# Performance work log

Hardware: AMD Instinct MI355X
Metric: run time of the kernel (lower is better)

The kernel has to match this reference:

```python
import jax, jax.numpy as jnp
import numpy as np

NUM_STUDENTS = 50000
NUM_PROBLEMS = 10000
EMBED_DIM = 64
NNZ = 3200000


def _spmm(rows, cols, vals, x, num_out):
    # out[r] = sum_{edges e with rows[e]==r} vals[e] * x[cols[e]]
    msgs = vals[:, None] * x[cols]  # [nnz, d]
    return jax.ops.segment_sum(msgs, rows, num_segments=num_out)


def setup_inputs() -> dict:
    key = jax.random.key(0)
    ks = jax.random.split(key, 8)
    return {
        "student_embeds": jax.random.normal(ks[0], (NUM_STUDENTS, EMBED_DIM), jnp.float32),
        "problem_embeds": jax.random.normal(ks[1], (NUM_PROBLEMS, EMBED_DIM), jnp.float32),
        "a_rows": jax.random.randint(ks[2], (NNZ,), 0, NUM_STUDENTS, jnp.int32),
        "a_cols": jax.random.randint(ks[3], (NNZ,), 0, NUM_PROBLEMS, jnp.int32),
        "a_vals": jax.random.uniform(ks[4], (NNZ,), jnp.float32),
        "ia_rows": jax.random.randint(ks[5], (NNZ,), 0, NUM_STUDENTS, jnp.int32),
        "ia_cols": jax.random.randint(ks[6], (NNZ,), 0, NUM_PROBLEMS, jnp.int32),
        "ia_vals": jax.random.uniform(ks[7], (NNZ,), jnp.float32),
    }


def reference(student_embeds, problem_embeds, a_rows, a_cols, a_vals,
              ia_rows, ia_cols, ia_vals):
    num_students = student_embeds.shape[0]
    num_problems = problem_embeds.shape[0]
    # a_matrix @ problem_embeds
    student_embeds_c = _spmm(a_rows, a_cols, a_vals, problem_embeds, num_students)
    # a_matrix.T @ student_embeds (swap roles of rows/cols)
    problem_embeds_c = _spmm(a_cols, a_rows, a_vals, student_embeds, num_problems)
    student_embeds_ic = _spmm(ia_rows, ia_cols, ia_vals, problem_embeds, num_students)
    problem_embeds_ic = _spmm(ia_cols, ia_rows, ia_vals, student_embeds, num_problems)
    return (student_embeds_c, student_embeds_ic, problem_embeds_c, problem_embeds_ic)
```

## Files before the change

kernel.cpp:

```cpp
#include <hip/hip_runtime.h>
#include <hip/hip_bf16.h>

#define NBMAX 256
#define TILE  4096
#define KPT   16
#define BINSMAX 512

__device__ __forceinline__ int seg8(unsigned r, unsigned mult8) {
    return (int)__umulhi(r, mult8);
}

__global__ __launch_bounds__(256) void hist_all(
        const int* __restrict__ k0, const int* __restrict__ k1,
        const int* __restrict__ k2, const int* __restrict__ k3,
        int* __restrict__ gcnt4, int nnz, int rsh_s, int rsh_p) {
    __shared__ int h[NBMAX];
    int dir = blockIdx.x & 3;
    const int* key = (dir == 0) ? k0 : (dir == 1) ? k1 : (dir == 2) ? k2 : k3;
    int rsh = (dir & 1) ? rsh_p : rsh_s;
    h[threadIdx.x] = 0;
    __syncthreads();
    int ch = blockIdx.x >> 2, nch = gridDim.x >> 2;
    for (int i = ch * 256 + threadIdx.x; i < nnz; i += nch * 256)
        atomicAdd(&h[key[i] >> rsh], 1);
    __syncthreads();
    int v = h[threadIdx.x];
    if (v) atomicAdd(&gcnt4[dir * NBMAX + threadIdx.x], v);
}

__global__ __launch_bounds__(256) void scan_all(
        const int* __restrict__ gcnt4, int* __restrict__ boffs4,
        int* __restrict__ bcur4, int nb_s, int nb_p, int nnz,
        int* __restrict__ offsE, int* __restrict__ offsO, int NS, int NP8) {
    __shared__ int tmp[NBMAX];
    int dir = blockIdx.x, tid = threadIdx.x;
    int nb = (dir & 1) ? nb_p : nb_s;
    int v = (tid < nb) ? gcnt4[dir * NBMAX + tid] : 0;
    tmp[tid] = v;
    __syncthreads();
    for (int off = 1; off < NBMAX; off <<= 1) {
        int t = (tid >= off) ? tmp[tid - off] : 0;
        __syncthreads();
        tmp[tid] += t;
        __syncthreads();
    }
    if (tid < nb) {
        int e = tmp[tid] - v;
        boffs4[dir * (NBMAX + 1) + tid] = e;
        bcur4[dir * NBMAX + tid] = e;
    }
    if (tid == 0) boffs4[dir * (NBMAX + 1) + nb] = nnz;
    if (dir == 0 && tid == 0) { offsE[NS] = nnz; offsO[NP8] = nnz; }
}

__global__ __launch_bounds__(256) void staged_scatter(
        const int* __restrict__ key, const int* __restrict__ other,
        const float* __restrict__ vals, int* __restrict__ cursor,
        uint2* __restrict__ edges, int nnz, int rsh) {
    __shared__ int lhist[NBMAX], lofs[NBMAX], lbase[NBMAX];
    __shared__ uint2 stage[TILE];
    __shared__ int   sslot[TILE];
    int tid = threadIdx.x;
    int lmask = (1 << rsh) - 1;
    int ntiles = (nnz + TILE - 1) / TILE;
    for (int tile = blockIdx.x; tile < ntiles; tile += gridDim.x) {
        int tbeg = tile * TILE;
        int n = nnz - tbeg; if (n > TILE) n = TILE;
        lhist[tid] = 0;
        __syncthreads();
        int myb[KPT], myr[KPT]; unsigned myo[KPT]; float myv[KPT];
        #pragma unroll
        for (int k = 0; k < KPT; ++k) {
            int s = k * 256 + tid;
            if (s < n) {
                int i = tbeg + s;
                int ky = key[i];
                myb[k] = ky >> rsh;
                myo[k] = (unsigned)other[i] | ((unsigned)(ky & lmask) << 16);
                myv[k] = vals[i];
                myr[k] = atomicAdd(&lhist[myb[k]], 1);
            } else myb[k] = -1;
        }
        __syncthreads();
        int h = lhist[tid];
        lofs[tid] = h;
        __syncthreads();
        for (int off = 1; off < NBMAX; off <<= 1) {
            int t = (tid >= off) ? lofs[tid - off] : 0;
            __syncthreads();
            lofs[tid] += t;
            __syncthreads();
        }
        lofs[tid] -= h;
        if (h > 0) lbase[tid] = atomicAdd(&cursor[tid], h);
        __syncthreads();
        #pragma unroll
        for (int k = 0; k < KPT; ++k) {
            if (myb[k] >= 0) {
                int ls = lofs[myb[k]] + myr[k];
                stage[ls] = make_uint2(myo[k], __float_as_uint(myv[k]));
                sslot[ls] = lbase[myb[k]] + myr[k];
            }
        }
        __syncthreads();
        #pragma unroll
        for (int k = 0; k < KPT; ++k) {
            int s = k * 256 + tid;
            if (s < n) edges[sslot[s]] = stage[s];
        }
        __syncthreads();
    }
}

__global__ __launch_bounds__(512) void row_scatter2(
        const uint2* __restrict__ e1, uint2* __restrict__ e2,
        const int* __restrict__ boffs, int* __restrict__ offs,
        int odd, int nb, int rsh, int nrows, unsigned mult8) {
    __shared__ int cnt[BINSMAX * 8];
    __shared__ int tot[512];
    __shared__ int lcur[BINSMAX];
    int tid = threadIdx.x;
    int g = blockIdx.x;
    int x = g & 7;
    int sk = (g >> 3) & 7;
    int bi = g >> 6;
    int b = x + 8 * bi;
    if (b >= nb) return;
    int bins = odd ? (8 << rsh) : (1 << rsh);
    int beg = boffs[b], end = boffs[b + 1];
    int len = end - beg;
    for (int i = tid; i < BINSMAX * 8; i += 512) cnt[i] = 0;
    __syncthreads();
    int per = (len + 7) >> 3;
    if (len > 0) {
        for (int i = beg + tid; i < end; i += 512) {
            uint2 e = e1[i];
            int lrow = (int)(e.x >> 16);
            int bin = odd ? (lrow * 8 + seg8(e.x & 0xFFFFu, mult8)) : lrow;
            int sl = (i - beg) / per;
            atomicAdd(&cnt[bin * 8 + sl], 1);
        }
    }
    __syncthreads();
    int own = 0;
    if (tid < bins) {
        #pragma unroll
        for (int j = 0; j < 8; ++j) own += cnt[tid * 8 + j];
    }
    tot[tid] = (tid < bins) ? own : 0;
    __syncthreads();
    for (int off = 1; off < 512; off <<= 1) {
        int t = (tid >= off) ? tot[tid - off] : 0;
        __syncthreads();
        tot[tid] += t;
        __syncthreads();
    }
    if (tid < bins) {
        int fineoff = tot[tid] - own;
        int basej = 0;
        for (int j = 0; j < sk; ++j) basej += cnt[tid * 8 + j];
        lcur[tid] = beg + fineoff + basej;
        if (sk == 0) {
            if (!odd) {
                int row = (b << rsh) + tid;
                if (row < nrows) offs[row] = beg + fineoff;
            } else {
                int row = (b << rsh) + (tid >> 3);
                if (row < nrows) offs[(row << 3) + (tid & 7)] = beg + fineoff;
            }
        }
    }
    __syncthreads();
    int lo = beg + sk * per;
    int hi = lo + per; if (hi > end) hi = end;
    for (int i = lo + tid; i < hi; i += 512) {
        uint2 e = e1[i];
        int lrow = (int)(e.x >> 16);
        int bin = odd ? (lrow * 8 + seg8(e.x & 0xFFFFu, mult8)) : lrow;
        int slot = atomicAdd(&lcur[bin], 1);
        e2[slot] = make_uint2(e.x & 0xFFFFu, e.y);
    }
}

__device__ __forceinline__ float4 gather_row4(
        int beg, int end, const uint2* __restrict__ edges,
        const float* __restrict__ x, int lane) {
    int q = lane >> 4, l16 = lane & 15;
    float4 acc = make_float4(0.f, 0.f, 0.f, 0.f);
    for (int base = beg; base < end; base += 64) {
        int n = end - base; if (n > 64) n = 64;
        uint2 e = make_uint2(0u, 0u);
        if (lane < n) e = edges[base + lane];
        for (int j = 0; j < n; j += 8) {
            int i0 = j + q, i1 = j + 4 + q;
            int   c0 = __shfl((int)e.x, i0);
            float v0 = __uint_as_float(__shfl((int)e.y, i0));
            int   c1 = __shfl((int)e.x, i1);
            float v1 = __uint_as_float(__shfl((int)e.y, i1));
            float4 x0 = *(const float4*)(x + (((size_t)c0) << 6) + (l16 << 2));
            float4 x1 = *(const float4*)(x + (((size_t)c1) << 6) + (l16 << 2));
            acc.x += v0 * x0.x; acc.y += v0 * x0.y;
            acc.z += v0 * x0.z; acc.w += v0 * x0.w;
            acc.x += v1 * x1.x; acc.y += v1 * x1.y;
            acc.z += v1 * x1.z; acc.w += v1 * x1.w;
        }
    }
    acc.x += __shfl_xor(acc.x, 16); acc.y += __shfl_xor(acc.y, 16);
    acc.z += __shfl_xor(acc.z, 16); acc.w += __shfl_xor(acc.w, 16);
    acc.x += __shfl_xor(acc.x, 32); acc.y += __shfl_xor(acc.y, 32);
    acc.z += __shfl_xor(acc.z, 32); acc.w += __shfl_xor(acc.w, 32);
    return acc;
}

__global__ __launch_bounds__(256) void row_gather(
        const int* __restrict__ offs, const uint2* __restrict__ edges,
        const float* __restrict__ x, float* __restrict__ out, int nrows) {
    int r = blockIdx.x * 4 + (threadIdx.x >> 6);
    int lane = threadIdx.x & 63;
    if (r >= nrows) return;
    float4 acc = gather_row4(offs[r], offs[r + 1], edges, x, lane);
    if ((lane >> 4) == 0)
        *(float4*)(out + (((size_t)r) << 6) + ((lane & 15) << 2)) = acc;
}

__global__ __launch_bounds__(256) void xcd_gather(
        const int* __restrict__ offs, const uint2* __restrict__ edges,
        const float* __restrict__ x, float* __restrict__ partial, int NP) {
    int g = blockIdx.x;
    int slot = g & 7;
    int t = g >> 3;
    int wave = threadIdx.x >> 6, lane = threadIdx.x & 63;
    int r = t * 4 + wave;
    if (r >= NP) return;
    int bin = r * 8 + slot;
    float4 acc = gather_row4(offs[bin], offs[bin + 1], edges, x, lane);
    if ((lane >> 4) == 0)
        *(float4*)(partial + (size_t)slot * NP * 64 + (((size_t)r) << 6) + ((lane & 15) << 2)) = acc;
}

__global__ __launch_bounds__(256) void reduce8(
        const float* __restrict__ partial, float* __restrict__ out, int n4) {
    int i = blockIdx.x * 256 + threadIdx.x;
    if (i < n4) {
        const float4* p = (const float4*)partial;
        float4 s = make_float4(0.f, 0.f, 0.f, 0.f);
        #pragma unroll
        for (int xx = 0; xx < 8; ++xx) {
            float4 v = p[(size_t)xx * n4 + i];
            s.x += v.x; s.y += v.y; s.z += v.z; s.w += v.w;
        }
        ((float4*)out)[i] = s;
    }
}

__global__ void spmm_scatter_kernel(const int* __restrict__ rows, const int* __restrict__ cols,
                                    const float* __restrict__ vals,
                                    const float* __restrict__ s_emb, const float* __restrict__ p_emb,
                                    float* __restrict__ out_s, float* __restrict__ out_p, int nnz) {
    long long t = (long long)blockIdx.x * blockDim.x + threadIdx.x;
    int e = (int)(t >> 6);
    int d = (int)(t & 63);
    if (e >= nnz) return;
    int r = rows[e];
    int c = cols[e];
    float v = vals[e];
    atomicAdd(&out_s[(size_t)r * 64 + d], v * p_emb[(size_t)c * 64 + d]);
    atomicAdd(&out_p[(size_t)c * 64 + d], v * s_emb[(size_t)r * 64 + d]);
}

extern "C" void kernel_launch(void* const* d_in, const int* in_sizes, int n_in,
                              void* d_out, int out_size, void* d_ws, size_t ws_size,
                              hipStream_t stream) {
    const float* s_emb   = (const float*)d_in[0];
    const float* p_emb   = (const float*)d_in[1];
    const int*   a_rows  = (const int*)d_in[2];
    const int*   a_cols  = (const int*)d_in[3];
    const float* a_vals  = (const float*)d_in[4];
    const int*   ia_rows = (const int*)d_in[5];
    const int*   ia_cols = (const int*)d_in[6];
    const float* ia_vals = (const float*)d_in[7];

    const int NS  = in_sizes[0] / 64;
    const int NP  = in_sizes[1] / 64;
    const int nnz = in_sizes[2];
    const int NP8 = NP * 8;

    float* out = (float*)d_out;
    float* out_sc  = out;
    float* out_sic = out_sc  + (size_t)NS * 64;
    float* out_pc  = out_sic + (size_t)NS * 64;
    float* out_pic = out_pc  + (size_t)NP * 64;

    int rsh_s = 0; while ((((long long)NS + (1LL << rsh_s) - 1) >> rsh_s) > NBMAX) rsh_s++;
    int rsh_p = 0; while ((((long long)NP + (1LL << rsh_p) - 1) >> rsh_p) > NBMAX) rsh_p++;
    int nb_s = (NS + (1 << rsh_s) - 1) >> rsh_s;
    int nb_p = (NP + (1 << rsh_p) - 1) >> rsh_p;
    unsigned mult8 = (unsigned)((8ULL << 32) / (unsigned)NS);

    const size_t edges_bytes = (size_t)nnz * sizeof(uint2);
    const size_t offsE_bytes = (size_t)(NS + 1) * sizeof(int);
    const size_t offsO_bytes = (size_t)(NP8 + 1) * sizeof(int);
    const size_t need = 2 * edges_bytes + offsE_bytes + offsO_bytes
                      + (size_t)(4 * NBMAX + 4 * (NBMAX + 1) + 4 * NBMAX) * sizeof(int) + 256;
    const bool packable = (NS <= 0xFFFF) && (NP <= 0xFFFF) &&
                          ((1 << rsh_s) <= BINSMAX) && ((8 << rsh_p) <= BINSMAX) &&
                          (edges_bytes >= (size_t)NP8 * 64 * sizeof(float)) &&
                          ((NP * 64) % 4 == 0);

    if (ws_size < need || !packable) {
        hipMemsetAsync(d_out, 0, (size_t)out_size * sizeof(float), stream);
        const long long total = (long long)nnz * 64;
        const int grid = (int)((total + 255) / 256);
        spmm_scatter_kernel<<<grid, 256, 0, stream>>>(a_rows, a_cols, a_vals, s_emb, p_emb,
                                                      out_sc, out_pc, nnz);
        spmm_scatter_kernel<<<grid, 256, 0, stream>>>(ia_rows, ia_cols, ia_vals, s_emb, p_emb,
                                                      out_sic, out_pic, nnz);
        return;
    }

    char* w = (char*)d_ws;
    uint2* edges1 = (uint2*)w;  w += edges_bytes;
    uint2* edges2 = (uint2*)w;  w += edges_bytes;
    int*   offsE  = (int*)w;    w += offsE_bytes;
    int*   offsO  = (int*)w;    w += offsO_bytes;
    int*   gcnt4  = (int*)w;    w += 4 * NBMAX * sizeof(int);
    int*   boffs4 = (int*)w;    w += 4 * (NBMAX + 1) * sizeof(int);
    int*   bcur4  = (int*)w;
    float* partial = (float*)edges1;

    hipMemsetAsync(gcnt4, 0, 4 * NBMAX * sizeof(int), stream);
    hist_all<<<1024, 256, 0, stream>>>(a_rows, a_cols, ia_rows, ia_cols,
                                       gcnt4, nnz, rsh_s, rsh_p);
    scan_all<<<4, 256, 0, stream>>>(gcnt4, boffs4, bcur4, nb_s, nb_p, nnz,
                                    offsE, offsO, NS, NP8);

    const int ntiles = (nnz + TILE - 1) / TILE;
    const int grid_rs_s = 64 * ((nb_s + 7) / 8);
    const int grid_rs_p = 64 * ((nb_p + 7) / 8);

    struct Dir { const int* key; const int* other; const float* vals;
                 float* out; int odd; };
    Dir dirs[4] = {
        { a_rows,  a_cols,  a_vals,  out_sc,  0 },
        { a_cols,  a_rows,  a_vals,  out_pc,  1 },
        { ia_rows, ia_cols, ia_vals, out_sic, 0 },
        { ia_cols, ia_rows, ia_vals, out_pic, 1 },
    };
    for (int t = 0; t < 4; ++t) {
        const Dir& D = dirs[t];
        if (!D.odd) {
            staged_scatter<<<ntiles, 256, 0, stream>>>(D.key, D.other, D.vals,
                                                       bcur4 + t * NBMAX, edges1, nnz, rsh_s);
            row_scatter2<<<grid_rs_s, 512, 0, stream>>>(edges1, edges2,
                                                        boffs4 + t * (NBMAX + 1), offsE,
                                                        0, nb_s, rsh_s, NS, mult8);
            row_gather<<<(NS + 3) / 4, 256, 0, stream>>>(offsE, edges2, p_emb, D.out, NS);
        } else {
            staged_scatter<<<ntiles, 256, 0, stream>>>(D.key, D.other, D.vals,
                                                       bcur4 + t * NBMAX, edges1, nnz, rsh_p);
            row_scatter2<<<grid_rs_p, 512, 0, stream>>>(edges1, edges2,
                                                        boffs4 + t * (NBMAX + 1), offsO,
                                                        1, nb_p, rsh_p, NP, mult8);
            xcd_gather<<<8 * ((NP + 3) / 4), 256, 0, stream>>>(offsO, edges2,
                                                               s_emb, partial, NP);
            reduce8<<<(NP * 64 / 4 + 255) / 256, 256, 0, stream>>>(partial, D.out, NP * 64 / 4);
        }
    }
}
```

Baseline: 647.3 us.

## Vectorize key loads, transpose row-scatter counters, fully unroll gather inner loop

The histogram and staged-scatter kernels now read keys, indices and values as int4/float4, with a scalar tail path for leftovers. This cuts the number of global load instructions. In row_scatter2 the counter array becomes slice-major with a padded stride, and the per-slice length is rounded up to a power of two so shifts replace the integer division. That can leave the eight slices unevenly loaded. The gather inner loop is fully unrolled over 64 edges, with padded zero-weight edges pointing at row 0, and the column offset is hoisted; short rows may then issue wasted loads.

Result: slower. 667.1 us (+3.1%).

```diff
diff --git a/kernel.cpp b/kernel.cpp
--- a/kernel.cpp
+++ b/kernel.cpp
@@ -5,6 +5,7 @@
 #define TILE  4096
 #define KPT   16
 #define BINSMAX 512
+#define SLP   520
 
 __device__ __forceinline__ int seg8(unsigned r, unsigned mult8) {
     return (int)__umulhi(r, mult8);
@@ -21,8 +22,18 @@
     h[threadIdx.x] = 0;
     __syncthreads();
     int ch = blockIdx.x >> 2, nch = gridDim.x >> 2;
-    for (int i = ch * 256 + threadIdx.x; i < nnz; i += nch * 256)
-        atomicAdd(&h[key[i] >> rsh], 1);
+    int nnz4 = nnz >> 2;
+    for (int i = ch * 256 + threadIdx.x; i < nnz4; i += nch * 256) {
+        int4 k4 = ((const int4*)key)[i];
+        atomicAdd(&h[k4.x >> rsh], 1);
+        atomicAdd(&h[k4.y >> rsh], 1);
+        atomicAdd(&h[k4.z >> rsh], 1);
+        atomicAdd(&h[k4.w >> rsh], 1);
+    }
+    if (ch == 0) {
+        for (int i = (nnz4 << 2) + threadIdx.x; i < nnz; i += 256)
+            atomicAdd(&h[key[i] >> rsh], 1);
+    }
     __syncthreads();
     int v = h[threadIdx.x];
     if (v) atomicAdd(&gcnt4[dir * NBMAX + threadIdx.x], v);
@@ -70,16 +81,39 @@
         __syncthreads();
         int myb[KPT], myr[KPT]; unsigned myo[KPT]; float myv[KPT];
         #pragma unroll
-        for (int k = 0; k < KPT; ++k) {
-            int s = k * 256 + tid;
-            if (s < n) {
+        for (int g = 0; g < 4; ++g) {
+            int s = g * 1024 + tid * 4;
+            if (s + 4 <= n) {
                 int i = tbeg + s;
-                int ky = key[i];
-                myb[k] = ky >> rsh;
-                myo[k] = (unsigned)other[i] | ((unsigned)(ky & lmask) << 16);
-                myv[k] = vals[i];
-                myr[k] = atomicAdd(&lhist[myb[k]], 1);
-            } else myb[k] = -1;
+                int4   k4 = *(const int4*)(key + i);
+                int4   o4 = *(const int4*)(other + i);
+                float4 v4 = *(const float4*)(vals + i);
+                int   kk[4] = {k4.x, k4.y, k4.z, k4.w};
+                int   oo[4] = {o4.x, o4.y, o4.z, o4.w};
+                float vv[4] = {v4.x, v4.y, v4.z, v4.w};
+                #pragma unroll
+                for (int k = 0; k < 4; ++k) {
+                    int m = g * 4 + k;
+                    myb[m] = kk[k] >> rsh;
+                    myo[m] = (unsigned)oo[k] | ((unsigned)(kk[k] & lmask) << 16);
+                    myv[m] = vv[k];
+                    myr[m] = atomicAdd(&lhist[myb[m]], 1);
+                }
+            } else {
+                #pragma unroll
+                for (int k = 0; k < 4; ++k) {
+                    int m = g * 4 + k;
+                    int s2 = s + k;
+                    if (s2 < n) {
+                        int i = tbeg + s2;
+                        int ky = key[i];
+                        myb[m] = ky >> rsh;
+                        myo[m] = (unsigned)other[i] | ((unsigned)(ky & lmask) << 16);
+                        myv[m] = vals[i];
+                        myr[m] = atomicAdd(&lhist[myb[m]], 1);
+                    } else myb[m] = -1;
+                }
+            }
         }
         __syncthreads();
         int h = lhist[tid];
@@ -116,7 +150,7 @@
         const uint2* __restrict__ e1, uint2* __restrict__ e2,
         const int* __restrict__ boffs, int* __restrict__ offs,
         int odd, int nb, int rsh, int nrows, unsigned mult8) {
-    __shared__ int cnt[BINSMAX * 8];
+    __shared__ int cnt[8 * SLP];
     __shared__ int tot[512];
     __shared__ int lcur[BINSMAX];
     int tid = threadIdx.x;
@@ -129,23 +163,27 @@
     int bins = odd ? (8 << rsh) : (1 << rsh);
     int beg = boffs[b], end = boffs[b + 1];
     int len = end - beg;
-    for (int i = tid; i < BINSMAX * 8; i += 512) cnt[i] = 0;
-    __syncthreads();
-    int per = (len + 7) >> 3;
+    for (int i = tid; i < 8 * SLP; i += 512) cnt[i] = 0;
+    __syncthreads();
+    int psh = 0;
+    {
+        int per = (len + 7) >> 3;
+        while ((1 << psh) < per) psh++;
+    }
     if (len > 0) {
         for (int i = beg + tid; i < end; i += 512) {
             uint2 e = e1[i];
             int lrow = (int)(e.x >> 16);
             int bin = odd ? (lrow * 8 + seg8(e.x & 0xFFFFu, mult8)) : lrow;
-            int sl = (i - beg) / per;
-            atomicAdd(&cnt[bin * 8 + sl], 1);
+            int sl = (i - beg) >> psh;
+            atomicAdd(&cnt[sl * SLP + bin], 1);
         }
     }
     __syncthreads();
     int own = 0;
     if (tid < bins) {
         #pragma unroll
-        for (int j = 0; j < 8; ++j) own += cnt[tid * 8 + j];
+        for (int j = 0; j < 8; ++j) own += cnt[j * SLP + tid];
     }
     tot[tid] = (tid < bins) ? own : 0;
     __syncthreads();
@@ -158,7 +196,7 @@
     if (tid < bins) {
         int fineoff = tot[tid] - own;
         int basej = 0;
-        for (int j = 0; j < sk; ++j) basej += cnt[tid * 8 + j];
+        for (int j = 0; j < sk; ++j) basej += cnt[j * SLP + tid];
         lcur[tid] = beg + fineoff + basej;
         if (sk == 0) {
             if (!odd) {
@@ -171,8 +209,8 @@
         }
     }
     __syncthreads();
-    int lo = beg + sk * per;
-    int hi = lo + per; if (hi > end) hi = end;
+    int lo = beg + (sk << psh);
+    int hi = lo + (1 << psh); if (hi > end) hi = end;
     for (int i = lo + tid; i < hi; i += 512) {
         uint2 e = e1[i];
         int lrow = (int)(e.x >> 16);
@@ -186,19 +224,20 @@
         int beg, int end, const uint2* __restrict__ edges,
         const float* __restrict__ x, int lane) {
     int q = lane >> 4, l16 = lane & 15;
+    const float* xq = x + (l16 << 2);
     float4 acc = make_float4(0.f, 0.f, 0.f, 0.f);
     for (int base = beg; base < end; base += 64) {
-        int n = end - base; if (n > 64) n = 64;
         uint2 e = make_uint2(0u, 0u);
-        if (lane < n) e = edges[base + lane];
-        for (int j = 0; j < n; j += 8) {
+        if (base + lane < end) e = edges[base + lane];
+        #pragma unroll
+        for (int j = 0; j < 64; j += 8) {
             int i0 = j + q, i1 = j + 4 + q;
             int   c0 = __shfl((int)e.x, i0);
             float v0 = __uint_as_float(__shfl((int)e.y, i0));
             int   c1 = __shfl((int)e.x, i1);
             float v1 = __uint_as_float(__shfl((int)e.y, i1));
-            float4 x0 = *(const float4*)(x + (((size_t)c0) << 6) + (l16 << 2));
-            float4 x1 = *(const float4*)(x + (((size_t)c1) << 6) + (l16 << 2));
+            float4 x0 = *(const float4*)(xq + (((size_t)c0) << 6));
+            float4 x1 = *(const float4*)(xq + (((size_t)c1) << 6));
             acc.x += v0 * x0.x; acc.y += v0 * x0.y;
             acc.z += v0 * x0.z; acc.w += v0 * x0.w;
             acc.x += v1 * x1.x; acc.y += v1 * x1.y;
```
